# Kernel tuning notes

Hardware: AMD Instinct MI355X
Metric: run time of the kernel (lower is better)

Reference implementation:

```python
import jax, jax.numpy as jnp
import numpy as np

DIM = 2048
N_HEADS = 16
HEAD_DIM = DIM // N_HEADS  # 128
B, T = 2, 4096
K_CONV = 4
EPS = 1e-5


def _silu(x):
    return x * jax.nn.sigmoid(x)


def _l2norm(x):
    return x * jax.lax.rsqrt(jnp.sum(x * x, axis=-1, keepdims=True) + 1e-6)


def _short_conv(x, w):
    # depthwise causal conv1d, kernel K, then SiLU. x: [B,T,D], w: [D,K]
    K = w.shape[1]
    xp = jnp.pad(x, ((0, 0), (K - 1, 0), (0, 0)))
    y = xp[:, 0:x.shape[1], :] * w[:, 0]
    for i in range(1, K):
        y = y + xp[:, i:i + x.shape[1], :] * w[:, i]
    return _silu(y)


def _delta_rule(q, k, v, beta):
    # DeltaNet recurrence (math-equivalent to fla chunk_delta_rule with
    # use_qk_l2norm_in_kernel=True and default scale Dk**-0.5).
    # q,k: [B,T,H,Dk]; v: [B,T,H,Dv]; beta: [B,T,H]
    Dk = q.shape[-1]
    q = _l2norm(q) * (Dk ** -0.5)
    k = _l2norm(k)
    qT = jnp.swapaxes(q, 0, 1)  # [T,B,H,Dk]
    kT = jnp.swapaxes(k, 0, 1)
    vT = jnp.swapaxes(v, 0, 1)
    bT = jnp.swapaxes(beta, 0, 1)  # [T,B,H]

    def step(S, inp):
        qt, kt, vt, bt = inp
        # prediction error u = v - S^T k
        u = vt - jnp.einsum('bhk,bhkv->bhv', kt, S)
        S = S + bt[:, :, None, None] * kt[..., :, None] * u[..., None, :]
        o = jnp.einsum('bhk,bhkv->bhv', qt, S)
        return S, o

    S0 = jnp.zeros(q.shape[0:1] + q.shape[2:4] + (v.shape[-1],), dtype=q.dtype)
    _, o = jax.lax.scan(step, S0, (qT, kT, vT, bT))
    return jnp.swapaxes(o, 0, 1)  # [B,T,H,Dv]


def _rmsnorm(x, w):
    var = jnp.mean(x * x, axis=-1, keepdims=True)
    return x * jax.lax.rsqrt(var + EPS) * w


def setup_inputs() -> dict:
    key = jax.random.key(0)
    ks = jax.random.split(key, 16)
    std = 0.02
    inp = {
        'hidden_states': jax.random.normal(ks[0], (B, T, DIM), jnp.float32),
        'k_cache': jax.random.normal(ks[1], (B, T, N_HEADS, HEAD_DIM), jnp.float32),
        'v_cache': jax.random.normal(ks[2], (B, T, N_HEADS, HEAD_DIM), jnp.float32),
        'cos': jax.random.normal(ks[3], (B, T, HEAD_DIM), jnp.float32),
        'sin': jax.random.normal(ks[4], (B, T, HEAD_DIM), jnp.float32),
        'Wq': jax.random.normal(ks[5], (DIM, DIM), jnp.float32) * std,
        'Wk': jax.random.normal(ks[6], (DIM, DIM), jnp.float32) * std,
        'Wv': jax.random.normal(ks[7], (DIM, DIM), jnp.float32) * std,
        'Wo': jax.random.normal(ks[8], (DIM, DIM), jnp.float32) * std,
        'Wg': jax.random.normal(ks[9], (DIM, DIM), jnp.float32) * std,
        'Wb': jax.random.normal(ks[10], (DIM, N_HEADS), jnp.float32) * std,
        'conv_wq': jax.random.normal(ks[11], (DIM, K_CONV), jnp.float32) * 0.3,
        'conv_wk': jax.random.normal(ks[12], (DIM, K_CONV), jnp.float32) * 0.3,
        'conv_wv': jax.random.normal(ks[13], (DIM, K_CONV), jnp.float32) * 0.3,
        'norm_w': jnp.ones((HEAD_DIM,), jnp.float32),
    }
    return inp


def reference(hidden_states, k_cache, v_cache, cos, sin,
              Wq, Wk, Wv, Wo, Wg, Wb, conv_wq, conv_wk, conv_wv, norm_w):
    # Deterministic eval path of CrossSwitcher (mode='random', not training,
    # q_len>64): conv -> delta rule -> RMSNorm -> sigmoid gate -> o_proj.
    b, t, d = hidden_states.shape
    q = hidden_states @ Wq
    k = hidden_states @ Wk
    v = hidden_states @ Wv
    q = _short_conv(q, conv_wq)
    k = _short_conv(k, conv_wk)
    v = _short_conv(v, conv_wv)
    q = q.reshape(b, t, N_HEADS, HEAD_DIM)
    k = k.reshape(b, t, N_HEADS, HEAD_DIM)
    v = v.reshape(b, t, N_HEADS, HEAD_DIM)
    beta = jax.nn.sigmoid(hidden_states @ Wb)  # [B,T,H]
    o = _delta_rule(q, k, v, beta)             # [B,T,H,Dh]
    o = _rmsnorm(o, norm_w)
    g = (hidden_states @ Wg).reshape(b, t, N_HEADS, HEAD_DIM)
    o = o * jax.nn.sigmoid(g)
    o = o.reshape(b, t, d) @ Wo
    return o
```

## Files before the change

### kernel.cpp

```cpp
#include <hip/hip_runtime.h>
#include <cstdint>
#include <cstddef>

#define DEVI __device__ __forceinline__

typedef __attribute__((ext_vector_type(8))) short short8;
typedef __attribute__((ext_vector_type(4))) float floatx4;

constexpr int B_ = 2, T_ = 4096, D_ = 2048, H_ = 16, DH = 128;
constexpr int BT = B_ * T_;
constexpr int C_ = 64, NC = T_ / C_;
constexpr int RSQ = 3 * D_;

DEVI float bf2f(ushort u){ union { uint32_t i; float f; } v; v.i = ((uint32_t)u) << 16; return v.f; }
DEVI ushort f2bf(float f){ union { float f; uint32_t i; } v; v.f = f; uint32_t r = v.i + 0x7fff + ((v.i >> 16) & 1); return (ushort)(r >> 16); }
DEVI float sigm(float x){ return 1.f / (1.f + __expf(-x)); }

DEVI void async_load16(const void* g, void* l){
  __builtin_amdgcn_global_load_lds((const __attribute__((address_space(1))) unsigned int*)g,
                                   (__attribute__((address_space(3))) unsigned int*)l, 16, 0, 0);
}
DEVI floatx4 mfma16(short8 a, short8 b, floatx4 c){
  return __builtin_amdgcn_mfma_f32_16x16x32_bf16(a, b, c, 0, 0, 0);
}

__global__ __launch_bounds__(256) void cast_bf16_kernel(const float* __restrict__ x,
                                                        ushort* __restrict__ y, int n){
  int i = (blockIdx.x * 256 + threadIdx.x) * 8;
  if (i + 8 <= n){
    floatx4 a = *(const floatx4*)(x + i);
    floatx4 b = *(const floatx4*)(x + i + 4);
    short8 o;
    o[0]=(short)f2bf(a[0]); o[1]=(short)f2bf(a[1]); o[2]=(short)f2bf(a[2]); o[3]=(short)f2bf(a[3]);
    o[4]=(short)f2bf(b[0]); o[5]=(short)f2bf(b[1]); o[6]=(short)f2bf(b[2]); o[7]=(short)f2bf(b[3]);
    *(short8*)(y + i) = o;
  }
}

__global__ __launch_bounds__(256) void transpose_cast_kernel(const float* __restrict__ w,
                                                             ushort* __restrict__ wt){
  __shared__ float tile[32][33];
  int bx = blockIdx.x, by = blockIdx.y;
  int tx = threadIdx.x & 31, ty = threadIdx.x >> 5;
  #pragma unroll
  for (int j = 0; j < 4; ++j)
    tile[ty + j*8][tx] = w[(size_t)(by*32 + ty + j*8) * D_ + bx*32 + tx];
  __syncthreads();
  #pragma unroll
  for (int j = 0; j < 4; ++j){
    int n = bx*32 + ty + j*8, k = by*32 + tx;
    wt[(size_t)n * D_ + k] = f2bf(tile[tx][ty + j*8]);
  }
}

__global__ __launch_bounds__(256) void cast_wbT(const float* __restrict__ Wb,
                                                ushort* __restrict__ WbT){
  int c = blockIdx.x * 256 + threadIdx.x;
  #pragma unroll
  for (int h = 0; h < H_; ++h)
    WbT[h * D_ + c] = f2bf(Wb[(size_t)c * H_ + h]);
}

template<bool F32OUT>
__global__ __launch_bounds__(512) void gemm256k(const ushort* __restrict__ A,
                                                const ushort* __restrict__ Bt,
                                                void* __restrict__ Cv,
                                                int M, int N, int K){
  __shared__ __align__(16) ushort As[2][256 * 64];
  __shared__ __align__(16) ushort Bs[2][256 * 64];
  const int tid = threadIdx.x;
  const int w = tid >> 6, lane = tid & 63, l16 = lane & 15, lq = lane >> 4;
  const int wm = w >> 2, wn = w & 3;
  const int xcd = (int)blockIdx.x & 7, j = (int)blockIdx.x >> 3;
  const int cpx = gridDim.x >> 3;
  const int ccols = cpx >> 3;
  const int bm = ((xcd & 3) << 3) + (j & 7);
  const int bn = (xcd >> 2) * ccols + (j >> 3);
  const int srow = tid >> 3;
  const int ce = ((tid & 7) ^ (srow & 7)) * 8;
  const ushort* Ab = A + (size_t)(bm*256 + srow) * K + ce;
  const ushort* Bb = Bt + (size_t)(bn*256 + srow) * K + ce;
  const int NT = K >> 6;

  floatx4 acc[8][4];
  #pragma unroll
  for (int i = 0; i < 8; ++i)
    #pragma unroll
    for (int jj = 0; jj < 4; ++jj) acc[i][jj] = (floatx4)0.f;

  auto stageA = [&](int kt, int buf){
    #pragma unroll
    for (int jj = 0; jj < 4; ++jj)
      async_load16(Ab + (size_t)(jj*64) * K + kt*64, (char*)&As[buf][0] + (jj*512 + tid)*16);
  };
  auto stageB = [&](int kt, int buf){
    #pragma unroll
    for (int jj = 0; jj < 4; ++jj)
      async_load16(Bb + (size_t)(jj*64) * K + kt*64, (char*)&Bs[buf][0] + (jj*512 + tid)*16);
  };
  auto frag = [&](const ushort* base, int row, int ks) -> short8 {
    int cB = (ks*64 + lq*16) ^ ((row & 7) << 4);
    return *(const short8*)(base + row*64 + (cB >> 1));
  };

  stageA(0, 0); stageB(0, 0);
  if (NT > 1){ stageA(1, 1); stageB(1, 1);
    asm volatile("s_waitcnt vmcnt(8)" ::: "memory");
  } else {
    asm volatile("s_waitcnt vmcnt(0)" ::: "memory");
  }
  __builtin_amdgcn_s_barrier();

  short8 afr[4][2], bfr[4][2];
  #pragma unroll 2
  for (int kt = 0; kt < NT; ++kt){
    const int buf = kt & 1;
    const ushort* pa = &As[buf][0];
    const ushort* pb = &Bs[buf][0];
    const bool st = (kt + 2 < NT);
    #pragma unroll
    for (int mf = 0; mf < 4; ++mf){
      afr[mf][0] = frag(pa, wm*128 + mf*16 + l16, 0);
      afr[mf][1] = frag(pa, wm*128 + mf*16 + l16, 1);
    }
    #pragma unroll
    for (int nf = 0; nf < 2; ++nf){
      bfr[nf][0] = frag(pb, wn*64 + nf*16 + l16, 0);
      bfr[nf][1] = frag(pb, wn*64 + nf*16 + l16, 1);
    }
    __builtin_amdgcn_sched_barrier(0);
    __builtin_amdgcn_s_barrier();
    asm volatile("s_waitcnt lgkmcnt(0)" ::: "memory");
    __builtin_amdgcn_sched_barrier(0);
    __builtin_amdgcn_s_setprio(1);
    #pragma unroll
    for (int mf = 0; mf < 4; ++mf)
      #pragma unroll
      for (int nf = 0; nf < 2; ++nf){
        acc[mf][nf] = mfma16(afr[mf][0], bfr[nf][0], acc[mf][nf]);
        acc[mf][nf] = mfma16(afr[mf][1], bfr[nf][1], acc[mf][nf]);
      }
    __builtin_amdgcn_s_setprio(0);
    __builtin_amdgcn_sched_barrier(0);
    __builtin_amdgcn_s_barrier();
    #pragma unroll
    for (int nf = 2; nf < 4; ++nf){
      bfr[nf][0] = frag(pb, wn*64 + nf*16 + l16, 0);
      bfr[nf][1] = frag(pb, wn*64 + nf*16 + l16, 1);
    }
    __builtin_amdgcn_sched_barrier(0);
    __builtin_amdgcn_s_barrier();
    asm volatile("s_waitcnt lgkmcnt(0)" ::: "memory");
    __builtin_amdgcn_sched_barrier(0);
    __builtin_amdgcn_s_setprio(1);
    #pragma unroll
    for (int mf = 0; mf < 4; ++mf)
      #pragma unroll
      for (int nf = 2; nf < 4; ++nf){
        acc[mf][nf] = mfma16(afr[mf][0], bfr[nf][0], acc[mf][nf]);
        acc[mf][nf] = mfma16(afr[mf][1], bfr[nf][1], acc[mf][nf]);
      }
    __builtin_amdgcn_s_setprio(0);
    __builtin_amdgcn_sched_barrier(0);
    __builtin_amdgcn_s_barrier();
    #pragma unroll
    for (int mf = 0; mf < 4; ++mf){
      afr[mf][0] = frag(pa, wm*128 + (mf + 4)*16 + l16, 0);
      afr[mf][1] = frag(pa, wm*128 + (mf + 4)*16 + l16, 1);
    }
    if (st) stageB(kt + 2, buf);
    __builtin_amdgcn_sched_barrier(0);
    __builtin_amdgcn_s_barrier();
    asm volatile("s_waitcnt lgkmcnt(0)" ::: "memory");
    __builtin_amdgcn_sched_barrier(0);
    __builtin_amdgcn_s_setprio(1);
    #pragma unroll
    for (int mf = 0; mf < 4; ++mf)
      #pragma unroll
      for (int nf = 2; nf < 4; ++nf){
        acc[mf + 4][nf] = mfma16(afr[mf][0], bfr[nf][0], acc[mf + 4][nf]);
        acc[mf + 4][nf] = mfma16(afr[mf][1], bfr[nf][1], acc[mf + 4][nf]);
      }
    __builtin_amdgcn_s_setprio(0);
    __builtin_amdgcn_sched_barrier(0);
    __builtin_amdgcn_s_barrier();
    if (st) stageA(kt + 2, buf);
    __builtin_amdgcn_sched_barrier(0);
    __builtin_amdgcn_s_barrier();
    __builtin_amdgcn_s_setprio(1);
    #pragma unroll
    for (int mf = 0; mf < 4; ++mf)
      #pragma unroll
      for (int nf = 0; nf < 2; ++nf){
        acc[mf + 4][nf] = mfma16(afr[mf][0], bfr[nf][0], acc[mf + 4][nf]);
        acc[mf + 4][nf] = mfma16(afr[mf][1], bfr[nf][1], acc[mf + 4][nf]);
      }
    __builtin_amdgcn_s_setprio(0);
    __builtin_amdgcn_sched_barrier(0);
    if (st)                   asm volatile("s_waitcnt vmcnt(8)" ::: "memory");
    else if (kt + 1 < NT)     asm volatile("s_waitcnt vmcnt(0)" ::: "memory");
    __builtin_amdgcn_s_barrier();
  }

  #pragma unroll
  for (int mf = 0; mf < 8; ++mf)
    #pragma unroll
    for (int nf = 0; nf < 4; ++nf)
      #pragma unroll
      for (int r = 0; r < 4; ++r){
        int row = bm*256 + wm*128 + mf*16 + lq*4 + r;
        int col = bn*256 + wn*64 + nf*16 + l16;
        if (F32OUT) ((float*)Cv)[(size_t)row * N + col] = acc[mf][nf][r];
        else        ((ushort*)Cv)[(size_t)row * N + col] = f2bf(acc[mf][nf][r]);
      }
}

__global__ __launch_bounds__(256) void conv3_kernel(
    const ushort* __restrict__ fqkv,
    const float* __restrict__ cwq, const float* __restrict__ cwk, const float* __restrict__ cwv,
    ushort* __restrict__ qn, ushort* __restrict__ kn, ushort* __restrict__ vc){
  const int blk = blockIdx.x;
  const int b  = (blk * 8) >> 12;
  const int t0 = (blk * 8) & (T_ - 1);
  const int tid = threadIdx.x;
  const int ch0 = tid * 8;

  const float*  cws[3]  = {cwq, cwk, cwv};
  ushort*       dsts[3] = {qn, kn, vc};

  #pragma unroll
  for (int s = 0; s < 3; ++s){
    const ushort* src = fqkv + s * D_;
    floatx4 w[8];
    #pragma unroll
    for (int j = 0; j < 8; ++j) w[j] = *(const floatx4*)&cws[s][(ch0 + j) * 4];

    float xf[11][8];
    #pragma unroll
    for (int idx = 0; idx < 11; ++idx){
      int t = t0 - 3 + idx;
      short8 x = (t >= 0) ? *(const short8*)(src + (size_t)(b*T_ + t)*RSQ + ch0)
                          : (short8)(short)0;
      #pragma unroll
      for (int j = 0; j < 8; ++j) xf[idx][j] = bf2f((ushort)x[j]);
    }

    #pragma unroll
    for (int tt = 0; tt < 8; ++tt){
      float y[8];
      #pragma unroll
      for (int j = 0; j < 8; ++j){
        float a = xf[tt][j]*w[j][0] + xf[tt+1][j]*w[j][1]
                + xf[tt+2][j]*w[j][2] + xf[tt+3][j]*w[j][3];
        y[j] = a * sigm(a);
      }
      float scale = 1.f;
      if (s < 2){
        float ss = 0.f;
        #pragma unroll
        for (int j = 0; j < 8; ++j) ss += y[j]*y[j];
        #pragma unroll
        for (int m = 1; m < 16; m <<= 1) ss += __shfl_xor(ss, m);
        scale = rsqrtf(ss + 1e-6f);
        if (s == 0) scale *= 0.08838834764831845f;
      }
      short8 o;
      #pragma unroll
      for (int j = 0; j < 8; ++j) o[j] = (short)f2bf(y[j] * scale);
      *(short8*)(dsts[s] + (size_t)(b*T_ + t0 + tt)*D_ + ch0) = o;
    }
  }
}

__global__ __launch_bounds__(256) void beta_kernel(const ushort* __restrict__ hb,
                                                   const ushort* __restrict__ WbT,
                                                   float* __restrict__ beta){
  const int r = blockIdx.x * 4 + (threadIdx.x >> 6);
  const int lane = threadIdx.x & 63;
  float xf[32];
  #pragma unroll
  for (int i = 0; i < 4; ++i){
    short8 x = *(const short8*)(hb + (size_t)r * D_ + i*512 + lane*8);
    #pragma unroll
    for (int j = 0; j < 8; ++j) xf[i*8 + j] = bf2f((ushort)x[j]);
  }
  float res = 0.f;
  #pragma unroll
  for (int h = 0; h < H_; ++h){
    float s = 0.f;
    #pragma unroll
    for (int i = 0; i < 4; ++i){
      short8 wv = *(const short8*)(WbT + (size_t)h * D_ + i*512 + lane*8);
      #pragma unroll
      for (int j = 0; j < 8; ++j) s += xf[i*8 + j] * bf2f((ushort)wv[j]);
    }
    #pragma unroll
    for (int m = 1; m < 64; m <<= 1) s += __shfl_xor(s, m);
    if (lane == h) res = s;
  }
  if (lane < H_) beta[(size_t)r * H_ + lane] = sigm(res);
}

__global__ __launch_bounds__(256) void phase1(
    const ushort* __restrict__ kn, const ushort* __restrict__ vc, const float* __restrict__ beta,
    ushort* __restrict__ Wneg, ushort* __restrict__ U, ushort* __restrict__ KTg){
  __shared__ __align__(16) char smem[72960];
  ushort* Ks = (ushort*)smem;
  ushort* Xb = (ushort*)smem;
  ushort* KT = (ushort*)(smem + 17408);
  ushort* VT = (ushort*)(smem + 17408 + 18432);
  ushort* Xt = (ushort*)(smem + 17408 + 36864);
  ushort* Pb = (ushort*)(smem + 17408 + 36864 + 9216);
  float*  bet = (float*)(smem + 17408 + 36864 + 18432);

  const int bx = blockIdx.x;
  const int c = bx & 63, h = (bx >> 6) & 15, b = bx >> 10;
  const int t0 = c * 64;
  const int tid = threadIdx.x, w = tid >> 6, lane = tid & 63, l16 = lane & 15, lq = lane >> 4;

  {
    int i = tid >> 2, d0 = (tid & 3) * 32;
    const ushort* kp = kn + (size_t)(b*T_ + t0 + i) * D_ + h*DH + d0;
    const ushort* vp = vc + (size_t)(b*T_ + t0 + i) * D_ + h*DH + d0;
    #pragma unroll
    for (int j = 0; j < 4; ++j){
      short8 kv = *(const short8*)(kp + j*8);
      short8 vv = *(const short8*)(vp + j*8);
      *(short8*)&Ks[i*136 + d0 + j*8] = kv;
      #pragma unroll
      for (int e = 0; e < 8; ++e){
        int d = d0 + j*8 + e;
        KT[d*72 + i] = (ushort)kv[e];
        VT[d*72 + i] = (ushort)vv[e];
      }
    }
    if (tid < 64) bet[tid] = beta[(size_t)(b*T_ + t0 + tid) * H_ + h];
  }
  __syncthreads();

  floatx4 accL[4];
  #pragma unroll
  for (int fn = 0; fn < 4; ++fn) accL[fn] = (floatx4)0.f;
  #pragma unroll
  for (int ks = 0; ks < 4; ++ks){
    short8 a = *(const short8*)&Ks[(w*16 + l16)*136 + ks*32 + lq*8];
    #pragma unroll
    for (int fn = 0; fn < 4; ++fn){
      short8 bb = *(const short8*)&Ks[(fn*16 + l16)*136 + ks*32 + lq*8];
      accL[fn] = mfma16(a, bb, accL[fn]);
    }
  }
  __syncthreads();

  {
    size_t kb = (size_t)bx * (128 * 64);
    int d = tid >> 1, i0 = (tid & 1) * 32;
    #pragma unroll
    for (int j = 0; j < 4; ++j)
      *(short8*)(KTg + kb + d*64 + i0 + j*8) = *(const short8*)&KT[d*72 + i0 + j*8];
  }

  #pragma unroll
  for (int fn = 0; fn < 4; ++fn)
    #pragma unroll
    for (int r = 0; r < 4; ++r){
      int i = w*16 + lq*4 + r, j = fn*16 + l16;
      float v = (j < i) ? (-bet[i] * accL[fn][r]) : 0.f;
      ushort vb = f2bf(v);
      Xb[i*72 + j] = vb;
      Xt[j*72 + i] = vb;
      Pb[i*72 + j] = (i == j) ? f2bf(1.f) : vb;
    }
  __syncthreads();

  #pragma unroll 1
  for (int s = 0; s < 5; ++s){
    floatx4 accY[4];
    #pragma unroll
    for (int fn = 0; fn < 4; ++fn) accY[fn] = (floatx4)0.f;
    #pragma unroll
    for (int ks = 0; ks < 2; ++ks){
      short8 a = *(const short8*)&Xb[(w*16 + l16)*72 + ks*32 + lq*8];
      #pragma unroll
      for (int fn = 0; fn < 4; ++fn){
        short8 bb = *(const short8*)&Xt[(fn*16 + l16)*72 + ks*32 + lq*8];
        accY[fn] = mfma16(a, bb, accY[fn]);
      }
    }
    __syncthreads();
    #pragma unroll
    for (int fn = 0; fn < 4; ++fn)
      #pragma unroll
      for (int r = 0; r < 4; ++r){
        int i = w*16 + lq*4 + r, n = fn*16 + l16;
        ushort v = f2bf(accY[fn][r]);
        Xb[i*72 + n] = v;
        Xt[n*72 + i] = v;
      }
    __syncthreads();
    floatx4 accP[4];
    #pragma unroll
    for (int fn = 0; fn < 4; ++fn)
      #pragma unroll
      for (int r = 0; r < 4; ++r)
        accP[fn][r] = bf2f(Pb[(w*16 + lq*4 + r)*72 + fn*16 + l16]);
    #pragma unroll
    for (int ks = 0; ks < 2; ++ks){
      short8 a = *(const short8*)&Pb[(w*16 + l16)*72 + ks*32 + lq*8];
      #pragma unroll
      for (int fn = 0; fn < 4; ++fn){
        short8 bb = *(const short8*)&Xt[(fn*16 + l16)*72 + ks*32 + lq*8];
        accP[fn] = mfma16(a, bb, accP[fn]);
      }
    }
    #pragma unroll
    for (int fn = 0; fn < 4; ++fn)
      #pragma unroll
      for (int r = 0; r < 4; ++r)
        Pb[(w*16 + lq*4 + r)*72 + fn*16 + l16] = f2bf(accP[fn][r]);
    __syncthreads();
  }

  floatx4 accW[8], accU[8];
  #pragma unroll
  for (int fn = 0; fn < 8; ++fn){ accW[fn] = (floatx4)0.f; accU[fn] = (floatx4)0.f; }
  #pragma unroll
  for (int ks = 0; ks < 2; ++ks){
    short8 p = *(const short8*)&Pb[(w*16 + l16)*72 + ks*32 + lq*8];
    short8 a;
    #pragma unroll
    for (int e = 0; e < 8; ++e)
      a[e] = (short)f2bf(bf2f((ushort)p[e]) * bet[ks*32 + lq*8 + e]);
    #pragma unroll
    for (int fn = 0; fn < 8; ++fn){
      short8 bk = *(const short8*)&KT[(fn*16 + l16)*72 + ks*32 + lq*8];
      short8 bv = *(const short8*)&VT[(fn*16 + l16)*72 + ks*32 + lq*8];
      accW[fn] = mfma16(a, bk, accW[fn]);
      accU[fn] = mfma16(a, bv, accU[fn]);
    }
  }
  size_t base = (size_t)bx * (64 * 128);
  #pragma unroll
  for (int fn = 0; fn < 8; ++fn)
    #pragma unroll
    for (int r = 0; r < 4; ++r){
      int i = w*16 + lq*4 + r, d = fn*16 + l16;
      Wneg[base + i*128 + d] = f2bf(-accW[fn][r]);
      U[base + i*128 + d]    = f2bf(accU[fn][r]);
    }
}

__global__ __launch_bounds__(256) void phase2(
    const ushort* __restrict__ qn, const ushort* __restrict__ KTg,
    const ushort* __restrict__ Wneg, const ushort* __restrict__ U,
    ushort* __restrict__ UpT, ushort* __restrict__ Opart){
  __shared__ __align__(16) ushort Sb[32 * 136];
  __shared__ __align__(16) ushort Ws[64 * 136];
  __shared__ __align__(16) ushort Qs[64 * 136];
  __shared__ __align__(16) ushort KTc[128 * 72];
  __shared__ __align__(16) ushort Us[64 * 40];
  __shared__ __align__(16) ushort UT[32 * 72];

  const int bx = blockIdx.x;
  const int xcd = bx & 7, j = bx >> 3;
  const int bh = xcd * 4 + (j >> 2), vs = j & 3;
  const int b = bh >> 4, h = bh & 15;
  const int tid = threadIdx.x, w = tid >> 6, lane = tid & 63, l16 = lane & 15, lq = lane >> 4;

  for (int e = tid; e < 32*136; e += 256) Sb[e] = 0;

  floatx4 M[2][2];
  #pragma unroll
  for (int nf = 0; nf < 2; ++nf)
    #pragma unroll
    for (int kf = 0; kf < 2; ++kf) M[nf][kf] = (floatx4)0.f;

  const int si = tid >> 2, sd = (tid & 3) * 32;
  short8 rW[4], rQ[4], rK[4], rU;

  auto loadr = [&](int c){
    size_t cb = ((size_t)(bh*NC + c)) * (64 * 128);
    const ushort* wp = Wneg + cb + si*128 + sd;
    const ushort* qp = qn + ((size_t)(b*T_ + c*64 + si)) * D_ + h*DH + sd;
    const ushort* kp = KTg + cb + tid*32;
    #pragma unroll
    for (int j2 = 0; j2 < 4; ++j2){
      rW[j2] = *(const short8*)(wp + j2*8);
      rQ[j2] = *(const short8*)(qp + j2*8);
      rK[j2] = *(const short8*)(kp + j2*8);
    }
    rU = *(const short8*)(U + cb + si*128 + vs*32 + (tid & 3)*8);
  };
  loadr(0);

  for (int c = 0; c < NC; ++c){
    #pragma unroll
    for (int j2 = 0; j2 < 4; ++j2){
      *(short8*)&Ws[si*136 + sd + j2*8] = rW[j2];
      *(short8*)&Qs[si*136 + sd + j2*8] = rQ[j2];
      *(short8*)&KTc[(tid >> 1)*72 + (tid & 1)*32 + j2*8] = rK[j2];
    }
    *(short8*)&Us[si*40 + (tid & 3)*8] = rU;
    __syncthreads();
    if (c + 1 < NC) loadr(c + 1);

    floatx4 accU[2];
    #pragma unroll
    for (int fn = 0; fn < 2; ++fn)
      #pragma unroll
      for (int r = 0; r < 4; ++r)
        accU[fn][r] = bf2f(Us[(w*16 + lq*4 + r)*40 + fn*16 + l16]);
    #pragma unroll
    for (int ks = 0; ks < 4; ++ks){
      short8 a = *(const short8*)&Ws[(w*16 + l16)*136 + ks*32 + lq*8];
      #pragma unroll
      for (int fn = 0; fn < 2; ++fn){
        short8 bs = *(const short8*)&Sb[(fn*16 + l16)*136 + ks*32 + lq*8];
        accU[fn] = mfma16(a, bs, accU[fn]);
      }
    }
    #pragma unroll
    for (int fn = 0; fn < 2; ++fn)
      #pragma unroll
      for (int r = 0; r < 4; ++r)
        UT[(fn*16 + l16)*72 + w*16 + lq*4 + r] = f2bf(accU[fn][r]);
    __syncthreads();

    size_t cb = ((size_t)(bh*NC + c)) * (64 * 128);
    {
      int nl = tid >> 3, i0 = (tid & 7) * 8;
      *(short8*)(UpT + cb + (size_t)(vs*32 + nl)*64 + i0) = *(const short8*)&UT[nl*72 + i0];
    }
    floatx4 accO[2];
    #pragma unroll
    for (int fn = 0; fn < 2; ++fn) accO[fn] = (floatx4)0.f;
    #pragma unroll
    for (int ks = 0; ks < 4; ++ks){
      short8 a = *(const short8*)&Qs[(w*16 + l16)*136 + ks*32 + lq*8];
      #pragma unroll
      for (int fn = 0; fn < 2; ++fn){
        short8 bs = *(const short8*)&Sb[(fn*16 + l16)*136 + ks*32 + lq*8];
        accO[fn] = mfma16(a, bs, accO[fn]);
      }
    }
    #pragma unroll
    for (int fn = 0; fn < 2; ++fn)
      #pragma unroll
      for (int r = 0; r < 4; ++r){
        int i = w*16 + lq*4 + r;
        Opart[cb + (size_t)i*128 + vs*32 + fn*16 + l16] = f2bf(accO[fn][r]);
      }
    #pragma unroll
    for (int ks = 0; ks < 2; ++ks){
      short8 a0 = *(const short8*)&UT[(l16)*72 + ks*32 + lq*8];
      short8 a1 = *(const short8*)&UT[(16 + l16)*72 + ks*32 + lq*8];
      #pragma unroll
      for (int kf = 0; kf < 2; ++kf){
        short8 bk = *(const short8*)&KTc[(w*32 + kf*16 + l16)*72 + ks*32 + lq*8];
        M[0][kf] = mfma16(a0, bk, M[0][kf]);
        M[1][kf] = mfma16(a1, bk, M[1][kf]);
      }
    }
    __syncthreads();
    #pragma unroll
    for (int nf = 0; nf < 2; ++nf)
      #pragma unroll
      for (int kf = 0; kf < 2; ++kf)
        #pragma unroll
        for (int r = 0; r < 4; ++r)
          Sb[(nf*16 + lq*4 + r)*136 + w*32 + kf*16 + l16] = f2bf(M[nf][kf][r]);
  }
}

__global__ __launch_bounds__(256) void phase3(
    const ushort* __restrict__ qn, const ushort* __restrict__ kn,
    const ushort* __restrict__ UpT, const ushort* __restrict__ Opart,
    const ushort* g, const float* __restrict__ norm_w,
    ushort* og){
  __shared__ __align__(16) ushort Qs[64 * 136];
  __shared__ __align__(16) ushort Ks[64 * 136];
  __shared__ __align__(16) ushort UTs[128 * 72];
  __shared__ __align__(16) ushort Os[64 * 136];
  __shared__ __align__(16) ushort Gs[64 * 136];
  __shared__ __align__(16) ushort Ab[64 * 72];
  __shared__ float nw[128];

  const int bx = blockIdx.x;
  const int c = bx & 63, h = (bx >> 6) & 15, b = bx >> 10;
  const int t0 = c * 64;
  const int tid = threadIdx.x, w = tid >> 6, lane = tid & 63, l16 = lane & 15, lq = lane >> 4;
  const size_t cb = (size_t)bx * (64 * 128);

  {
    int i = tid >> 2, d0 = (tid & 3) * 32;
    const ushort* qp = qn + (size_t)(b*T_ + t0 + i) * D_ + h*DH + d0;
    const ushort* kp = kn + (size_t)(b*T_ + t0 + i) * D_ + h*DH + d0;
    const ushort* gp = g  + (size_t)(b*T_ + t0 + i) * D_ + h*DH + d0;
    const ushort* op = Opart + cb + i*128 + d0;
    #pragma unroll
    for (int j = 0; j < 4; ++j){
      *(short8*)&Qs[i*136 + d0 + j*8] = *(const short8*)(qp + j*8);
      *(short8*)&Ks[i*136 + d0 + j*8] = *(const short8*)(kp + j*8);
      *(short8*)&Gs[i*136 + d0 + j*8] = *(const short8*)(gp + j*8);
      *(short8*)&Os[i*136 + d0 + j*8] = *(const short8*)(op + j*8);
    }
    int n = tid >> 1, i0 = (tid & 1) * 32;
    #pragma unroll
    for (int j = 0; j < 4; ++j)
      *(short8*)&UTs[n*72 + i0 + j*8] = *(const short8*)(UpT + cb + n*64 + i0 + j*8);
    if (tid < 128) nw[tid] = norm_w[tid];
  }
  __syncthreads();

  floatx4 accA[4];
  #pragma unroll
  for (int fn = 0; fn < 4; ++fn) accA[fn] = (floatx4)0.f;
  #pragma unroll
  for (int ks = 0; ks < 4; ++ks){
    short8 a = *(const short8*)&Qs[(w*16 + l16)*136 + ks*32 + lq*8];
    #pragma unroll
    for (int fn = 0; fn < 4; ++fn){
      short8 bb = *(const short8*)&Ks[(fn*16 + l16)*136 + ks*32 + lq*8];
      accA[fn] = mfma16(a, bb, accA[fn]);
    }
  }
  #pragma unroll
  for (int fn = 0; fn < 4; ++fn)
    #pragma unroll
    for (int r = 0; r < 4; ++r){
      int i = w*16 + lq*4 + r, j = fn*16 + l16;
      Ab[i*72 + j] = f2bf((j <= i) ? accA[fn][r] : 0.f);
    }
  __syncthreads();

  floatx4 accO[8];
  #pragma unroll
  for (int fn = 0; fn < 8; ++fn)
    #pragma unroll
    for (int r = 0; r < 4; ++r)
      accO[fn][r] = bf2f(Os[(w*16 + lq*4 + r)*136 + fn*16 + l16]);
  #pragma unroll
  for (int ks = 0; ks < 2; ++ks){
    short8 a = *(const short8*)&Ab[(w*16 + l16)*72 + ks*32 + lq*8];
    #pragma unroll
    for (int fn = 0; fn < 8; ++fn){
      short8 bu = *(const short8*)&UTs[(fn*16 + l16)*72 + ks*32 + lq*8];
      accO[fn] = mfma16(a, bu, accO[fn]);
    }
  }
  #pragma unroll
  for (int r = 0; r < 4; ++r){
    float ss = 0.f;
    #pragma unroll
    for (int fn = 0; fn < 8; ++fn) ss += accO[fn][r] * accO[fn][r];
    #pragma unroll
    for (int m = 1; m < 16; m <<= 1) ss += __shfl_xor(ss, m);
    float rms = rsqrtf(ss * (1.f / 128.f) + 1e-5f);
    int i = w*16 + lq*4 + r;
    #pragma unroll
    for (int fn = 0; fn < 8; ++fn){
      int d = fn*16 + l16;
      float gv = bf2f(Gs[i*136 + d]);
      float o = accO[fn][r] * rms * nw[d] * sigm(gv);
      og[(size_t)(b*T_ + t0 + i) * D_ + h*DH + d] = f2bf(o);
    }
  }
}

extern "C" void kernel_launch(void* const* d_in, const int* in_sizes, int n_in,
                              void* d_out, int out_size, void* d_ws, size_t ws_size,
                              hipStream_t stream){
  const float* hidden = (const float*)d_in[0];
  const float* Wq = (const float*)d_in[5];
  const float* Wk = (const float*)d_in[6];
  const float* Wv = (const float*)d_in[7];
  const float* Wo = (const float*)d_in[8];
  const float* Wg = (const float*)d_in[9];
  const float* Wb = (const float*)d_in[10];
  const float* cwq = (const float*)d_in[11];
  const float* cwk = (const float*)d_in[12];
  const float* cwv = (const float*)d_in[13];
  const float* nw  = (const float*)d_in[14];

  char* ws = (char*)d_ws;
  size_t off = 0;
  auto alloc = [&](size_t bytes){ void* p = ws + off; off += (bytes + 255) & ~(size_t)255; return p; };
  const size_t SZ = (size_t)BT * D_ * 2;
  ushort* hb   = (ushort*)alloc(SZ);
  ushort* wqT  = (ushort*)alloc((size_t)D_*D_*2);
  ushort* wkT  = (ushort*)alloc((size_t)D_*D_*2);
  ushort* wvT  = (ushort*)alloc((size_t)D_*D_*2);
  ushort* wgT  = (ushort*)alloc((size_t)D_*D_*2);
  ushort* woT  = (ushort*)alloc((size_t)D_*D_*2);
  ushort* wbT  = (ushort*)alloc((size_t)H_*D_*2);
  ushort* fqkv = (ushort*)alloc(3*SZ);
  ushort* kn   = (ushort*)alloc(SZ);
  ushort* vcv  = (ushort*)alloc(SZ);
  float*  beta = (float*)alloc((size_t)BT * H_ * 4);
  (void)in_sizes; (void)n_in; (void)out_size;
  if (off > ws_size) return;

  ushort* qn  = (ushort*)d_out;
  ushort* KTg = (ushort*)d_out + (size_t)BT * D_;

  cast_bf16_kernel<<<8192, 256, 0, stream>>>(hidden, hb, BT * D_);
  dim3 tg(64, 64);
  transpose_cast_kernel<<<tg, 256, 0, stream>>>(Wq, wqT);
  transpose_cast_kernel<<<tg, 256, 0, stream>>>(Wk, wkT);
  transpose_cast_kernel<<<tg, 256, 0, stream>>>(Wv, wvT);
  transpose_cast_kernel<<<tg, 256, 0, stream>>>(Wg, wgT);
  transpose_cast_kernel<<<tg, 256, 0, stream>>>(Wo, woT);
  cast_wbT<<<D_/256, 256, 0, stream>>>(Wb, wbT);

  {
    const int NWG = (BT / 256) * (RSQ / 256);
    gemm256k<false><<<NWG, 512, 0, stream>>>(hb, wqT, fqkv, BT, RSQ, D_);
  }

  conv3_kernel<<<BT/8, 256, 0, stream>>>(fqkv, cwq, cwk, cwv, qn, kn, vcv);
  beta_kernel<<<BT/4, 256, 0, stream>>>(hb, wbT, beta);

  ushort* gpre = fqkv;
  ushort* Wneg = fqkv + (size_t)BT * D_;
  ushort* Ubuf = fqkv + (size_t)2 * BT * D_;
  {
    const int NWG = (BT / 256) * (D_ / 256);
    gemm256k<false><<<NWG, 512, 0, stream>>>(hb, wgT, gpre, BT, D_, D_);
  }

  ushort* Opart = hb;

  phase1<<<B_ * H_ * NC, 256, 0, stream>>>(kn, vcv, beta, Wneg, Ubuf, KTg);
  ushort* UpT = vcv;
  phase2<<<B_ * H_ * 4, 256, 0, stream>>>(qn, KTg, Wneg, Ubuf, UpT, Opart);
  ushort* og = gpre;
  phase3<<<B_ * H_ * NC, 256, 0, stream>>>(qn, kn, UpT, Opart, gpre, nw, og);

  {
    const int NWG = (BT / 256) * (D_ / 256);
    gemm256k<true><<<NWG, 512, 0, stream>>>(og, woT, (float*)d_out, BT, D_, D_);
  }
}
```

Before: 727.4 us.

## Restructure GEMM main loop into two-stage software pipeline with fragment prefetch

Rewrites the 256x256 bf16 GEMM K-loop so each iteration processes two K-tiles. LDS fragment reads for the next phase are issued before or alongside the current MFMA block rather than after a barrier and lgkmcnt(0) wait. Split B-fragment registers (bf01/bf23) and a reordered MFMA quadrant sequence let LDS reads for the next tile overlap with compute, and the explicit lgkmcnt waits are dropped. It assumes NT is even and at least 2, and relies on the compiler to insert the correct LDS waits, which risks subtle hazards or register pressure.

```diff
diff --git a/kernel.cpp b/kernel.cpp
--- a/kernel.cpp
+++ b/kernel.cpp
@@ -61,6 +61,27 @@
     WbT[h * D_ + c] = f2bf(Wb[(size_t)c * H_ + h]);
 }
 
+#define GSB __builtin_amdgcn_sched_barrier(0)
+#define GBAR __builtin_amdgcn_s_barrier()
+#define RD_ALO(PA) { _Pragma("unroll") for (int mf = 0; mf < 4; ++mf){ \
+    af[mf][0] = frag(PA, wm*128 + mf*16 + l16, 0); \
+    af[mf][1] = frag(PA, wm*128 + mf*16 + l16, 1); } }
+#define RD_AHI(PA) { _Pragma("unroll") for (int mf = 0; mf < 4; ++mf){ \
+    af[mf][0] = frag(PA, wm*128 + (mf+4)*16 + l16, 0); \
+    af[mf][1] = frag(PA, wm*128 + (mf+4)*16 + l16, 1); } }
+#define RD_B01(PB) { _Pragma("unroll") for (int nf = 0; nf < 2; ++nf){ \
+    bf01[nf][0] = frag(PB, wn*64 + nf*16 + l16, 0); \
+    bf01[nf][1] = frag(PB, wn*64 + nf*16 + l16, 1); } }
+#define RD_B23(PB) { _Pragma("unroll") for (int nf = 0; nf < 2; ++nf){ \
+    bf23[nf][0] = frag(PB, wn*64 + (nf+2)*16 + l16, 0); \
+    bf23[nf][1] = frag(PB, wn*64 + (nf+2)*16 + l16, 1); } }
+#define MFMA_BLK(MO, NO, BF) { _Pragma("unroll") for (int mf = 0; mf < 4; ++mf){ \
+    _Pragma("unroll") for (int nf = 0; nf < 2; ++nf){ \
+      acc[(MO)+mf][(NO)+nf] = mfma16(af[mf][0], BF[nf][0], acc[(MO)+mf][(NO)+nf]); \
+      acc[(MO)+mf][(NO)+nf] = mfma16(af[mf][1], BF[nf][1], acc[(MO)+mf][(NO)+nf]); } } }
+#define PH_HEAD GSB; GBAR; GSB; __builtin_amdgcn_s_setprio(1)
+#define PH_TAIL __builtin_amdgcn_s_setprio(0)
+
 template<bool F32OUT>
 __global__ __launch_bounds__(512) void gemm256k(const ushort* __restrict__ A,
                                                 const ushort* __restrict__ Bt,
@@ -71,11 +92,11 @@
   const int tid = threadIdx.x;
   const int w = tid >> 6, lane = tid & 63, l16 = lane & 15, lq = lane >> 4;
   const int wm = w >> 2, wn = w & 3;
-  const int xcd = (int)blockIdx.x & 7, j = (int)blockIdx.x >> 3;
+  const int xcd = (int)blockIdx.x & 7, jb = (int)blockIdx.x >> 3;
   const int cpx = gridDim.x >> 3;
   const int ccols = cpx >> 3;
-  const int bm = ((xcd & 3) << 3) + (j & 7);
-  const int bn = (xcd >> 2) * ccols + (j >> 3);
+  const int bm = ((xcd & 3) << 3) + (jb & 7);
+  const int bn = (xcd >> 2) * ccols + (jb >> 3);
   const int srow = tid >> 3;
   const int ce = ((tid & 7) ^ (srow & 7)) * 8;
   const ushort* Ab = A + (size_t)(bm*256 + srow) * K + ce;
@@ -103,103 +124,49 @@
     return *(const short8*)(base + row*64 + (cB >> 1));
   };
 
+  short8 af[4][2], bf01[2][2], bf23[2][2];
+
   stageA(0, 0); stageB(0, 0);
-  if (NT > 1){ stageA(1, 1); stageB(1, 1);
-    asm volatile("s_waitcnt vmcnt(8)" ::: "memory");
-  } else {
-    asm volatile("s_waitcnt vmcnt(0)" ::: "memory");
-  }
-  __builtin_amdgcn_s_barrier();
-
-  short8 afr[4][2], bfr[4][2];
-  #pragma unroll 2
-  for (int kt = 0; kt < NT; ++kt){
-    const int buf = kt & 1;
-    const ushort* pa = &As[buf][0];
-    const ushort* pb = &Bs[buf][0];
+  stageA(1, 1); stageB(1, 1);
+  asm volatile("s_waitcnt vmcnt(8)" ::: "memory");
+  GBAR;
+  {
+    const ushort* pa = &As[0][0]; const ushort* pb = &Bs[0][0];
+    RD_ALO(pa); RD_B01(pb); RD_B23(pb);
+  }
+
+  #pragma unroll 1
+  for (int p = 0; p < NT / 2; ++p){
+    const int kt = 2 * p;
     const bool st = (kt + 2 < NT);
-    #pragma unroll
-    for (int mf = 0; mf < 4; ++mf){
-      afr[mf][0] = frag(pa, wm*128 + mf*16 + l16, 0);
-      afr[mf][1] = frag(pa, wm*128 + mf*16 + l16, 1);
-    }
-    #pragma unroll
-    for (int nf = 0; nf < 2; ++nf){
-      bfr[nf][0] = frag(pb, wn*64 + nf*16 + l16, 0);
-      bfr[nf][1] = frag(pb, wn*64 + nf*16 + l16, 1);
-    }
-    __builtin_amdgcn_sched_barrier(0);
-    __builtin_amdgcn_s_barrier();
-    asm volatile("s_waitcnt lgkmcnt(0)" ::: "memory");
-    __builtin_amdgcn_sched_barrier(0);
-    __builtin_amdgcn_s_setprio(1);
-    #pragma unroll
-    for (int mf = 0; mf < 4; ++mf)
-      #pragma unroll
-      for (int nf = 0; nf < 2; ++nf){
-        acc[mf][nf] = mfma16(afr[mf][0], bfr[nf][0], acc[mf][nf]);
-        acc[mf][nf] = mfma16(afr[mf][1], bfr[nf][1], acc[mf][nf]);
-      }
-    __builtin_amdgcn_s_setprio(0);
-    __builtin_amdgcn_sched_barrier(0);
-    __builtin_amdgcn_s_barrier();
-    #pragma unroll
-    for (int nf = 2; nf < 4; ++nf){
-      bfr[nf][0] = frag(pb, wn*64 + nf*16 + l16, 0);
-      bfr[nf][1] = frag(pb, wn*64 + nf*16 + l16, 1);
-    }
-    __builtin_amdgcn_sched_barrier(0);
-    __builtin_amdgcn_s_barrier();
-    asm volatile("s_waitcnt lgkmcnt(0)" ::: "memory");
-    __builtin_amdgcn_sched_barrier(0);
-    __builtin_amdgcn_s_setprio(1);
-    #pragma unroll
-    for (int mf = 0; mf < 4; ++mf)
-      #pragma unroll
-      for (int nf = 2; nf < 4; ++nf){
-        acc[mf][nf] = mfma16(afr[mf][0], bfr[nf][0], acc[mf][nf]);
-        acc[mf][nf] = mfma16(afr[mf][1], bfr[nf][1], acc[mf][nf]);
-      }
-    __builtin_amdgcn_s_setprio(0);
-    __builtin_amdgcn_sched_barrier(0);
-    __builtin_amdgcn_s_barrier();
-    #pragma unroll
-    for (int mf = 0; mf < 4; ++mf){
-      afr[mf][0] = frag(pa, wm*128 + (mf + 4)*16 + l16, 0);
-      afr[mf][1] = frag(pa, wm*128 + (mf + 4)*16 + l16, 1);
-    }
-    if (st) stageB(kt + 2, buf);
-    __builtin_amdgcn_sched_barrier(0);
-    __builtin_amdgcn_s_barrier();
-    asm volatile("s_waitcnt lgkmcnt(0)" ::: "memory");
-    __builtin_amdgcn_sched_barrier(0);
-    __builtin_amdgcn_s_setprio(1);
-    #pragma unroll
-    for (int mf = 0; mf < 4; ++mf)
-      #pragma unroll
-      for (int nf = 2; nf < 4; ++nf){
-        acc[mf + 4][nf] = mfma16(afr[mf][0], bfr[nf][0], acc[mf + 4][nf]);
-        acc[mf + 4][nf] = mfma16(afr[mf][1], bfr[nf][1], acc[mf + 4][nf]);
-      }
-    __builtin_amdgcn_s_setprio(0);
-    __builtin_amdgcn_sched_barrier(0);
-    __builtin_amdgcn_s_barrier();
-    if (st) stageA(kt + 2, buf);
-    __builtin_amdgcn_sched_barrier(0);
-    __builtin_amdgcn_s_barrier();
-    __builtin_amdgcn_s_setprio(1);
-    #pragma unroll
-    for (int mf = 0; mf < 4; ++mf)
-      #pragma unroll
-      for (int nf = 0; nf < 2; ++nf){
-        acc[mf + 4][nf] = mfma16(afr[mf][0], bfr[nf][0], acc[mf + 4][nf]);
-        acc[mf + 4][nf] = mfma16(afr[mf][1], bfr[nf][1], acc[mf + 4][nf]);
-      }
-    __builtin_amdgcn_s_setprio(0);
-    __builtin_amdgcn_sched_barrier(0);
-    if (st)                   asm volatile("s_waitcnt vmcnt(8)" ::: "memory");
-    else if (kt + 1 < NT)     asm volatile("s_waitcnt vmcnt(0)" ::: "memory");
-    __builtin_amdgcn_s_barrier();
+    const ushort* pa0 = &As[0][0]; const ushort* pb0 = &Bs[0][0];
+    const ushort* pa1 = &As[1][0]; const ushort* pb1 = &Bs[1][0];
+
+    PH_HEAD; MFMA_BLK(0, 0, bf01); PH_TAIL; GSB; GBAR;
+    PH_HEAD; MFMA_BLK(0, 2, bf23); PH_TAIL; GSB; GBAR;
+    RD_AHI(pa0);
+    if (st) stageB(kt + 2, 0);
+    PH_HEAD; MFMA_BLK(4, 2, bf23); PH_TAIL;
+    if (st) asm volatile("s_waitcnt vmcnt(4)" ::: "memory");
+    else    asm volatile("s_waitcnt vmcnt(0)" ::: "memory");
+    GSB; GBAR;
+    if (st) stageA(kt + 2, 0);
+    RD_B23(pb1);
+    PH_HEAD; MFMA_BLK(4, 0, bf01); PH_TAIL;
+    RD_ALO(pa1); RD_B01(pb1);
+    GSB; GBAR;
+
+    PH_HEAD; MFMA_BLK(0, 2, bf23); PH_TAIL; GSB; GBAR;
+    PH_HEAD; MFMA_BLK(0, 0, bf01); PH_TAIL; GSB; GBAR;
+    RD_AHI(pa1);
+    if (st) stageB(kt + 3, 1);
+    PH_HEAD; MFMA_BLK(4, 0, bf01); PH_TAIL;
+    if (st) asm volatile("s_waitcnt vmcnt(4)" ::: "memory");
+    GSB; GBAR;
+    if (st){ stageA(kt + 3, 1); RD_B01(pb0); }
+    PH_HEAD; MFMA_BLK(4, 2, bf23); PH_TAIL;
+    if (st){ RD_ALO(pa0); RD_B23(pb0); }
+    GSB; GBAR;
   }
 
   #pragma unroll
```

New measurement: 732.8 us. No clear change (+0.7%).
